# Kernel optimization log

Measured on AMD Instinct MI355X. Metric: run time of the kernel, lower is better.

## Reference

```python
import jax, jax.numpy as jnp
import numpy as np

DIM = 16
HID = 128
B = 1024
STEPS = 10  # RK4 steps in differentiable_forward


def setup_inputs() -> dict:
    key = jax.random.key(0)
    ks = jax.random.split(key, 8)

    def lin(k, fan_in, fan_out):
        return jax.random.normal(k, (fan_in, fan_out), jnp.float32) / np.float32(np.sqrt(fan_in))

    W0 = lin(ks[0], DIM + 1, HID)
    W1 = lin(ks[1], HID, HID)
    W2 = lin(ks[2], HID, HID)
    W3 = lin(ks[3], HID, HID)
    W4 = lin(ks[4], HID, DIM)
    b0 = jnp.zeros((HID,), jnp.float32)
    b1 = jnp.zeros((HID,), jnp.float32)
    b2 = jnp.zeros((HID,), jnp.float32)
    b3 = jnp.zeros((HID,), jnp.float32)
    b4 = jnp.zeros((DIM,), jnp.float32)
    x = jax.random.normal(ks[5], (B, DIM), jnp.float32)
    x_star = jax.random.normal(ks[6], (B, DIM), jnp.float32)
    return dict(x=x, x_star=x_star, W0=W0, b0=b0, W1=W1, b1=b1,
                W2=W2, b2=b2, W3=W3, b3=b3, W4=W4, b4=b4)


def reference(x, x_star, W0, b0, W1, b1, W2, b2, W3, b3, W4, b4):
    dtype = x.dtype

    def vel(t, z):
        # z: [..., DIM]; append scalar time channel -> [..., DIM+1]
        tcol = jnp.full(z.shape[:-1] + (1,), t, dtype)
        h = jnp.concatenate([z, tcol], axis=-1)
        h = jnp.tanh(h @ W0 + b0)
        h = jnp.tanh(h @ W1 + b1)
        h = jnp.tanh(h @ W2 + b2)
        h = jnp.tanh(h @ W3 + b3)
        return h @ W4 + b4

    def flow(z):
        # RK4 integration of the velocity field from t=0 to t=1 (10 steps)
        dt = 1.0 / STEPS
        for i in range(STEPS):
            t = i * dt
            k1 = vel(t, z)
            k2 = vel(t + 0.5 * dt, z + 0.5 * dt * k1)
            k3 = vel(t + 0.5 * dt, z + 0.5 * dt * k2)
            k4 = vel(t + dt, z + dt * k3)
            z = z + (k1 + 2.0 * k2 + 2.0 * k3 + k4) * (dt / 6.0)
        return z

    n = x.shape[0]
    y_comb = flow(jnp.concatenate([x, x_star], axis=0))
    y, y_star = y_comb[:n], y_comb[n:]

    diff = y - y_star
    norm = jnp.linalg.norm(diff, axis=1, keepdims=True) + 1e-8
    grad_phi_y = diff / norm  # [B, DIM]

    # Per-sample Jacobian J[b, i, j] = d y_i / d x_j (flow is pointwise per row)
    J = jax.vmap(jax.jacfwd(flow))(x)  # [B, DIM, DIM]

    G = jnp.einsum('bij,bik->bjk', J, J)  # J^T J
    G_inv = jnp.linalg.inv(G + 1e-6 * jnp.eye(DIM, dtype=dtype))
    grad_phi_x = jnp.einsum('bij,bi->bj', J, grad_phi_y)  # J^T grad_phi_y
    x_dot = -jnp.einsum('bjk,bk->bj', G_inv, grad_phi_x)
    return x_dot
```

## Files before the change

### kernel.cpp

```cpp
#include <hip/hip_runtime.h>
#include <math.h>

typedef _Float16 half8  __attribute__((ext_vector_type(8)));
typedef _Float16 half4  __attribute__((ext_vector_type(4)));
typedef float    float4v __attribute__((ext_vector_type(4)));

#define NDIM   16
#define HID    128
#define NSTEP  10
#define RPW    2
#define NROWS  48
#define XSTR   136
#define XISTR  40
#define SBS    17

__device__ __forceinline__ float tanh_fast(float v) {
  float e = __expf(2.f * v);
  return 1.f - 2.f * __builtin_amdgcn_rcpf(e + 1.f);
}

template<int CTRL>
__device__ __forceinline__ float qbcast(float v) {
  int i = __builtin_amdgcn_update_dpp(0, __builtin_bit_cast(int, v), CTRL, 0xF, 0xF, true);
  return __builtin_bit_cast(float, i);
}

__device__ __forceinline__ int oneuron(int c) {
  return 32*(c >> 5) + 16*((c >> 2) & 1) + 4*((c >> 3) & 3) + (c & 3);
}

__global__ __launch_bounds__(256, 2)
void flow_ode_kernel(const float* __restrict__ gx,  const float* __restrict__ gxs,
                     const float* __restrict__ W0,  const float* __restrict__ b0,
                     const float* __restrict__ W1,  const float* __restrict__ b1,
                     const float* __restrict__ W2,  const float* __restrict__ b2,
                     const float* __restrict__ W3,  const float* __restrict__ b3,
                     const float* __restrict__ W4,  const float* __restrict__ b4,
                     float* __restrict__ out)
{
  __shared__ __align__(16) _Float16 XT[2][NROWS][XSTR];
  __shared__ __align__(16) _Float16 XI[NROWS][XISTR];
  __shared__ float SbL[NROWS][SBS];

  const int tid  = threadIdx.x;
  const int mi   = tid >> 6;
  const int lane = tid & 63;
  const int q    = lane >> 4;
  const int ln   = lane & 15;
  const int g0   = blockIdx.x * RPW;

  half8 A0[2];
  half8 A1[2][4], A2[2][4], A3[2][4];
  half8 A4[4];
  float bw[4][2][4];
  float b4r[4];

  #pragma unroll
  for (int mt = 0; mt < 2; ++mt) {
    const int m = 16*(2*mi + mt) + ln;
    #pragma unroll
    for (int j = 0; j < 8; ++j) {
      const int k = 8*q + j;
      A0[mt][j] = (k < NDIM+1) ? (_Float16)W0[k*HID + m] : (_Float16)0.f;
    }
    #pragma unroll
    for (int ks = 0; ks < 4; ++ks) {
      #pragma unroll
      for (int j = 0; j < 8; ++j) {
        const int k = oneuron(32*ks + 8*q + j);
        A1[mt][ks][j] = (_Float16)W1[k*HID + m];
        A2[mt][ks][j] = (_Float16)W2[k*HID + m];
        A3[mt][ks][j] = (_Float16)W3[k*HID + m];
      }
    }
  }
  #pragma unroll
  for (int ks = 0; ks < 4; ++ks)
    #pragma unroll
    for (int j = 0; j < 8; ++j)
      A4[ks][j] = (_Float16)W4[oneuron(32*ks + 8*q + j)*NDIM + ln];

  #pragma unroll
  for (int mt = 0; mt < 2; ++mt)
    #pragma unroll
    for (int r = 0; r < 4; ++r) {
      const int m = 16*(2*mi + mt) + 4*q + r;
      bw[0][mt][r] = b0[m];
      bw[1][mt][r] = b1[m];
      bw[2][mt][r] = b2[m];
      bw[3][mt][r] = b3[m];
    }
  #pragma unroll
  for (int r = 0; r < 4; ++r) b4r[r] = b4[4*q + r];

  float sbr[4], sar[4];
  if (mi == 0) {
    const int p = ln & 3;
    const float* src = (p < 2) ? (gx + (g0 + p)*NDIM) : (gxs + (g0 + p - 2)*NDIM);
    #pragma unroll
    for (int r = 0; r < 4; ++r) sbr[r] = src[4*q + r];
  } else {
    #pragma unroll
    for (int r = 0; r < 4; ++r) sbr[r] = (ln == 4*q + r) ? 1.f : 0.f;
  }
  #pragma unroll
  for (int r = 0; r < 4; ++r) sar[r] = 0.f;

  for (int idx = tid; idx < NROWS*32; idx += 256)
    XI[idx >> 5][idx & 31] = (_Float16)0.f;
  __syncthreads();
  if (mi < 3) {
    half4 x4;
    #pragma unroll
    for (int r = 0; r < 4; ++r) x4[r] = (_Float16)sbr[r];
    *(half4*)&XI[mi*16 + ln][4*q] = x4;
  }
  __syncthreads();

  if (blockIdx.x & 1) __builtin_amdgcn_s_sleep(22);

  const float dt = 1.f / NSTEP;

  auto finish = [&](float4v (&D)[2][3], int wb) {
    float ss[2][4];
    half8 hh;
    #pragma unroll
    for (int mt = 0; mt < 2; ++mt)
      #pragma unroll
      for (int r = 0; r < 4; ++r) {
        const float h = tanh_fast(D[mt][0][r]);
        hh[4*mt + r] = (_Float16)h;
        ss[mt][r] = 1.f - h*h;
      }
    *(half8*)&XT[wb][ln][32*mi + 8*q] = hh;
    half8 t1, t2;
    #pragma unroll
    for (int mt = 0; mt < 2; ++mt)
      #pragma unroll
      for (int r = 0; r < 4; ++r) {
        t1[4*mt + r] = (_Float16)(D[mt][1][r] * qbcast<0x00>(ss[mt][r]));
        t2[4*mt + r] = (_Float16)(D[mt][2][r] * qbcast<0x55>(ss[mt][r]));
      }
    *(half8*)&XT[wb][16 + ln][32*mi + 8*q] = t1;
    *(half8*)&XT[wb][32 + ln][32*mi + 8*q] = t2;
    __syncthreads();
  };

  auto mid_layer = [&](const half8 (&A)[2][4], const float (&bb)[2][4], int rb, int wb) {
    float4v D[2][3];
    #pragma unroll
    for (int mt = 0; mt < 2; ++mt)
      #pragma unroll
      for (int nt = 0; nt < 3; ++nt)
        #pragma unroll
        for (int e = 0; e < 4; ++e) D[mt][nt][e] = (nt == 0) ? bb[mt][e] : 0.f;
    #pragma unroll
    for (int ks = 0; ks < 4; ++ks) {
      half8 Bf[3];
      #pragma unroll
      for (int nt = 0; nt < 3; ++nt)
        Bf[nt] = *(const half8*)&XT[rb][nt*16 + ln][32*ks + 8*q];
      #pragma unroll
      for (int nt = 0; nt < 3; ++nt) {
        D[0][nt] = __builtin_amdgcn_mfma_f32_16x16x32_f16(A[0][ks], Bf[nt], D[0][nt], 0, 0, 0);
        D[1][nt] = __builtin_amdgcn_mfma_f32_16x16x32_f16(A[1][ks], Bf[nt], D[1][nt], 0, 0, 0);
      }
    }
    finish(D, wb);
  };

  #pragma unroll 1
  for (int step = 0; step < NSTEP; ++step) {
    const float t0 = step * dt;
    #pragma unroll
    for (int stage = 0; stage < 4; ++stage) {
      {
        float4v D[2][3];
        #pragma unroll
        for (int mt = 0; mt < 2; ++mt)
          #pragma unroll
          for (int nt = 0; nt < 3; ++nt)
            #pragma unroll
            for (int e = 0; e < 4; ++e) D[mt][nt][e] = (nt == 0) ? bw[0][mt][e] : 0.f;
        half8 Bf[3];
        #pragma unroll
        for (int nt = 0; nt < 3; ++nt)
          Bf[nt] = *(const half8*)&XI[nt*16 + ln][8*q];
        #pragma unroll
        for (int nt = 0; nt < 3; ++nt) {
          D[0][nt] = __builtin_amdgcn_mfma_f32_16x16x32_f16(A0[0], Bf[nt], D[0][nt], 0, 0, 0);
          D[1][nt] = __builtin_amdgcn_mfma_f32_16x16x32_f16(A0[1], Bf[nt], D[1][nt], 0, 0, 0);
        }
        finish(D, 0);
      }
      mid_layer(A1, bw[1], 0, 1);
      mid_layer(A2, bw[2], 1, 0);
      mid_layer(A3, bw[3], 0, 1);
      {
        if (mi < 3) {
          float4v Da;
          #pragma unroll
          for (int e = 0; e < 4; ++e) Da[e] = (mi == 0) ? b4r[e] : 0.f;
          #pragma unroll
          for (int ks = 0; ks < 4; ++ks) {
            half8 Ba = *(const half8*)&XT[1][mi*16 + ln][32*ks + 8*q];
            Da = __builtin_amdgcn_mfma_f32_16x16x32_f16(A4[ks], Ba, Da, 0, 0, 0);
          }
          const float c_s = (stage < 2) ? 0.5f*dt : dt;
          half4 xn;
          if (stage < 3) {
            const float w_s = (stage == 0) ? 1.f : 2.f;
            #pragma unroll
            for (int r = 0; r < 4; ++r) {
              sar[r] += w_s * Da[r];
              xn[r] = (_Float16)(sbr[r] + c_s * Da[r]);
            }
          } else {
            #pragma unroll
            for (int r = 0; r < 4; ++r) {
              const float nb = sbr[r] + (dt * (1.f/6.f)) * (sar[r] + Da[r]);
              sbr[r] = nb;
              sar[r] = 0.f;
              xn[r] = (_Float16)nb;
            }
          }
          *(half4*)&XI[mi*16 + ln][4*q] = xn;
          if (mi == 0 && q == 0)
            XI[ln][16] = (_Float16)(t0 + ((stage < 2) ? 0.5f*dt : dt));
        }
        __syncthreads();
      }
    }
  }

  if (mi < 3) {
    #pragma unroll
    for (int r = 0; r < 4; ++r)
      SbL[mi*16 + ln][4*q + r] = sbr[r];
  }
  __syncthreads();

  if (mi < RPW) {
    const int p    = mi;
    const int jj   = ln;
    const int base = lane & 48;
    float c[NDIM], gv[NDIM], G[NDIM];
    #pragma unroll
    for (int i = 0; i < NDIM; ++i) c[i] = SbL[16 + 16*p + jj][i];
    float n2 = 0.f;
    #pragma unroll
    for (int i = 0; i < NDIM; ++i) {
      gv[i] = SbL[p][i] - SbL[2 + p][i];
      n2 += gv[i]*gv[i];
    }
    const float rinv = 1.f / (sqrtf(n2) + 1e-8f);
    float rhs = 0.f;
    #pragma unroll
    for (int i = 0; i < NDIM; ++i) rhs += c[i] * gv[i];
    rhs *= rinv;
    #pragma unroll
    for (int k = 0; k < NDIM; ++k) {
      float acc = (k == jj) ? 1e-6f : 0.f;
      #pragma unroll
      for (int i = 0; i < NDIM; ++i)
        acc += c[i] * __shfl(c[i], base + k, 64);
      G[k] = acc;
    }
    #pragma unroll
    for (int k = 0; k < NDIM-1; ++k) {
      const float piv  = __shfl(G[k], base + k, 64);
      const float prhs = __shfl(rhs,  base + k, 64);
      const float f = (jj > k) ? G[k] / piv : 0.f;
      #pragma unroll
      for (int cc = k; cc < NDIM; ++cc)
        G[cc] -= f * __shfl(G[cc], base + k, 64);
      rhs -= f * prhs;
    }
    float sol = 0.f;
    #pragma unroll
    for (int k = NDIM-1; k >= 0; --k) {
      const float piv = __shfl(G[k], base + k, 64);
      const float pr  = __shfl(rhs,  base + k, 64);
      const float xk  = pr / piv;
      if (jj == k) sol = xk;
      if (jj <  k) rhs -= G[k] * xk;
    }
    if (lane < NDIM)
      out[(g0 + p)*NDIM + jj] = -sol;
  }
}

extern "C" void kernel_launch(void* const* d_in, const int* in_sizes, int n_in,
                              void* d_out, int out_size, void* d_ws, size_t ws_size,
                              hipStream_t stream) {
  (void)in_sizes; (void)n_in; (void)d_ws; (void)ws_size; (void)out_size;
  flow_ode_kernel<<<dim3(512), dim3(256), 0, stream>>>(
      (const float*)d_in[0],  (const float*)d_in[1],
      (const float*)d_in[2],  (const float*)d_in[3],
      (const float*)d_in[4],  (const float*)d_in[5],
      (const float*)d_in[6],  (const float*)d_in[7],
      (const float*)d_in[8],  (const float*)d_in[9],
      (const float*)d_in[10], (const float*)d_in[11],
      (float*)d_out);
}
```

Measured before the change: 238.1 us.

## Halve block to two waves, each wave computing two neuron slices

Each block now runs 128 threads (two wavefronts) instead of four. Each wave holds weights for two 32-neuron slices and issues twice as many MFMAs per layer, and the per-wave state vectors are doubled to match. This reduces barrier participants and per-block LDS contention, and lets the B-fragment LDS reads be shared across more MFMAs. In exchange it roughly doubles weight registers per wave (launch bounds set to 128,1), which may cause spills or lower occupancy and serialises more work per wave.

```diff
diff --git a/kernel.cpp b/kernel.cpp
--- a/kernel.cpp
+++ b/kernel.cpp
@@ -29,7 +29,7 @@
   return 32*(c >> 5) + 16*((c >> 2) & 1) + 4*((c >> 3) & 3) + (c & 3);
 }
 
-__global__ __launch_bounds__(256, 2)
+__global__ __launch_bounds__(128, 1)
 void flow_ode_kernel(const float* __restrict__ gx,  const float* __restrict__ gxs,
                      const float* __restrict__ W0,  const float* __restrict__ b0,
                      const float* __restrict__ W1,  const float* __restrict__ b1,
@@ -49,28 +49,40 @@
   const int ln   = lane & 15;
   const int g0   = blockIdx.x * RPW;
 
-  half8 A0[2];
-  half8 A1[2][4], A2[2][4], A3[2][4];
+  half8 A0[2][2];
+  half8 A1[2][2][4], A2[2][2][4], A3[2][2][4];
   half8 A4[4];
-  float bw[4][2][4];
+  float bw[4][2][2][4];
   float b4r[4];
 
   #pragma unroll
-  for (int mt = 0; mt < 2; ++mt) {
-    const int m = 16*(2*mi + mt) + ln;
-    #pragma unroll
-    for (int j = 0; j < 8; ++j) {
-      const int k = 8*q + j;
-      A0[mt][j] = (k < NDIM+1) ? (_Float16)W0[k*HID + m] : (_Float16)0.f;
-    }
-    #pragma unroll
-    for (int ks = 0; ks < 4; ++ks) {
+  for (int h = 0; h < 2; ++h) {
+    const int v = 2*mi + h;
+    #pragma unroll
+    for (int mt = 0; mt < 2; ++mt) {
+      const int m = 16*(2*v + mt) + ln;
       #pragma unroll
       for (int j = 0; j < 8; ++j) {
-        const int k = oneuron(32*ks + 8*q + j);
-        A1[mt][ks][j] = (_Float16)W1[k*HID + m];
-        A2[mt][ks][j] = (_Float16)W2[k*HID + m];
-        A3[mt][ks][j] = (_Float16)W3[k*HID + m];
+        const int k = 8*q + j;
+        A0[h][mt][j] = (k < NDIM+1) ? (_Float16)W0[k*HID + m] : (_Float16)0.f;
+      }
+      #pragma unroll
+      for (int ks = 0; ks < 4; ++ks) {
+        #pragma unroll
+        for (int j = 0; j < 8; ++j) {
+          const int k = oneuron(32*ks + 8*q + j);
+          A1[h][mt][ks][j] = (_Float16)W1[k*HID + m];
+          A2[h][mt][ks][j] = (_Float16)W2[k*HID + m];
+          A3[h][mt][ks][j] = (_Float16)W3[k*HID + m];
+        }
+      }
+      #pragma unroll
+      for (int r = 0; r < 4; ++r) {
+        const int mm = 16*(2*v + mt) + 4*q + r;
+        bw[0][h][mt][r] = b0[mm];
+        bw[1][h][mt][r] = b1[mm];
+        bw[2][h][mt][r] = b2[mm];
+        bw[3][h][mt][r] = b3[mm];
       }
     }
   }
@@ -79,41 +91,42 @@
     #pragma unroll
     for (int j = 0; j < 8; ++j)
       A4[ks][j] = (_Float16)W4[oneuron(32*ks + 8*q + j)*NDIM + ln];
-
-  #pragma unroll
-  for (int mt = 0; mt < 2; ++mt)
-    #pragma unroll
-    for (int r = 0; r < 4; ++r) {
-      const int m = 16*(2*mi + mt) + 4*q + r;
-      bw[0][mt][r] = b0[m];
-      bw[1][mt][r] = b1[m];
-      bw[2][mt][r] = b2[m];
-      bw[3][mt][r] = b3[m];
-    }
   #pragma unroll
   for (int r = 0; r < 4; ++r) b4r[r] = b4[4*q + r];
 
-  float sbr[4], sar[4];
+  float sbr[2][4], sar[2][4];
   if (mi == 0) {
     const int p = ln & 3;
     const float* src = (p < 2) ? (gx + (g0 + p)*NDIM) : (gxs + (g0 + p - 2)*NDIM);
     #pragma unroll
-    for (int r = 0; r < 4; ++r) sbr[r] = src[4*q + r];
+    for (int r = 0; r < 4; ++r) {
+      sbr[0][r] = src[4*q + r];
+      sbr[1][r] = (ln == 4*q + r) ? 1.f : 0.f;
+    }
   } else {
     #pragma unroll
-    for (int r = 0; r < 4; ++r) sbr[r] = (ln == 4*q + r) ? 1.f : 0.f;
-  }
-  #pragma unroll
-  for (int r = 0; r < 4; ++r) sar[r] = 0.f;
-
-  for (int idx = tid; idx < NROWS*32; idx += 256)
+    for (int r = 0; r < 4; ++r) {
+      sbr[0][r] = (ln == 4*q + r) ? 1.f : 0.f;
+      sbr[1][r] = 0.f;
+    }
+  }
+  #pragma unroll
+  for (int h = 0; h < 2; ++h)
+    #pragma unroll
+    for (int r = 0; r < 4; ++r) sar[h][r] = 0.f;
+
+  for (int idx = tid; idx < NROWS*32; idx += 128)
     XI[idx >> 5][idx & 31] = (_Float16)0.f;
   __syncthreads();
-  if (mi < 3) {
-    half4 x4;
-    #pragma unroll
-    for (int r = 0; r < 4; ++r) x4[r] = (_Float16)sbr[r];
-    *(half4*)&XI[mi*16 + ln][4*q] = x4;
+  #pragma unroll
+  for (int h = 0; h < 2; ++h) {
+    const int v = 2*mi + h;
+    if (v < 3) {
+      half4 x4;
+      #pragma unroll
+      for (int r = 0; r < 4; ++r) x4[r] = (_Float16)sbr[h][r];
+      *(half4*)&XI[v*16 + ln][4*q] = x4;
+    }
   }
   __syncthreads();
 
@@ -121,39 +134,45 @@
 
   const float dt = 1.f / NSTEP;
 
-  auto finish = [&](float4v (&D)[2][3], int wb) {
-    float ss[2][4];
-    half8 hh;
-    #pragma unroll
-    for (int mt = 0; mt < 2; ++mt)
-      #pragma unroll
-      for (int r = 0; r < 4; ++r) {
-        const float h = tanh_fast(D[mt][0][r]);
-        hh[4*mt + r] = (_Float16)h;
-        ss[mt][r] = 1.f - h*h;
-      }
-    *(half8*)&XT[wb][ln][32*mi + 8*q] = hh;
-    half8 t1, t2;
-    #pragma unroll
-    for (int mt = 0; mt < 2; ++mt)
-      #pragma unroll
-      for (int r = 0; r < 4; ++r) {
-        t1[4*mt + r] = (_Float16)(D[mt][1][r] * qbcast<0x00>(ss[mt][r]));
-        t2[4*mt + r] = (_Float16)(D[mt][2][r] * qbcast<0x55>(ss[mt][r]));
-      }
-    *(half8*)&XT[wb][16 + ln][32*mi + 8*q] = t1;
-    *(half8*)&XT[wb][32 + ln][32*mi + 8*q] = t2;
+  auto finish = [&](float4v (&D)[2][2][3], int wb) {
+    #pragma unroll
+    for (int h = 0; h < 2; ++h) {
+      const int v = 2*mi + h;
+      float ss[2][4];
+      half8 hh;
+      #pragma unroll
+      for (int mt = 0; mt < 2; ++mt)
+        #pragma unroll
+        for (int r = 0; r < 4; ++r) {
+          const float hv = tanh_fast(D[h][mt][0][r]);
+          hh[4*mt + r] = (_Float16)hv;
+          ss[mt][r] = 1.f - hv*hv;
+        }
+      *(half8*)&XT[wb][ln][32*v + 8*q] = hh;
+      half8 t1, t2;
+      #pragma unroll
+      for (int mt = 0; mt < 2; ++mt)
+        #pragma unroll
+        for (int r = 0; r < 4; ++r) {
+          t1[4*mt + r] = (_Float16)(D[h][mt][1][r] * qbcast<0x00>(ss[mt][r]));
+          t2[4*mt + r] = (_Float16)(D[h][mt][2][r] * qbcast<0x55>(ss[mt][r]));
+        }
+      *(half8*)&XT[wb][16 + ln][32*v + 8*q] = t1;
+      *(half8*)&XT[wb][32 + ln][32*v + 8*q] = t2;
+    }
     __syncthreads();
   };
 
-  auto mid_layer = [&](const half8 (&A)[2][4], const float (&bb)[2][4], int rb, int wb) {
-    float4v D[2][3];
-    #pragma unroll
-    for (int mt = 0; mt < 2; ++mt)
-      #pragma unroll
-      for (int nt = 0; nt < 3; ++nt)
-        #pragma unroll
-        for (int e = 0; e < 4; ++e) D[mt][nt][e] = (nt == 0) ? bb[mt][e] : 0.f;
+  auto mid_layer = [&](const half8 (&A)[2][2][4], const float (&bb)[2][2][4], int rb, int wb) {
+    float4v D[2][2][3];
+    #pragma unroll
+    for (int h = 0; h < 2; ++h)
+      #pragma unroll
+      for (int mt = 0; mt < 2; ++mt)
+        #pragma unroll
+        for (int nt = 0; nt < 3; ++nt)
+          #pragma unroll
+          for (int e = 0; e < 4; ++e) D[h][mt][nt][e] = (nt == 0) ? bb[h][mt][e] : 0.f;
     #pragma unroll
     for (int ks = 0; ks < 4; ++ks) {
       half8 Bf[3];
@@ -161,10 +180,12 @@
       for (int nt = 0; nt < 3; ++nt)
         Bf[nt] = *(const half8*)&XT[rb][nt*16 + ln][32*ks + 8*q];
       #pragma unroll
-      for (int nt = 0; nt < 3; ++nt) {
-        D[0][nt] = __builtin_amdgcn_mfma_f32_16x16x32_f16(A[0][ks], Bf[nt], D[0][nt], 0, 0, 0);
-        D[1][nt] = __builtin_amdgcn_mfma_f32_16x16x32_f16(A[1][ks], Bf[nt], D[1][nt], 0, 0, 0);
-      }
+      for (int h = 0; h < 2; ++h)
+        #pragma unroll
+        for (int mt = 0; mt < 2; ++mt)
+          #pragma unroll
+          for (int nt = 0; nt < 3; ++nt)
+            D[h][mt][nt] = __builtin_amdgcn_mfma_f32_16x16x32_f16(A[h][mt][ks], Bf[nt], D[h][mt][nt], 0, 0, 0);
     }
     finish(D, wb);
   };
@@ -175,72 +196,84 @@
     #pragma unroll
     for (int stage = 0; stage < 4; ++stage) {
       {
-        float4v D[2][3];
-        #pragma unroll
-        for (int mt = 0; mt < 2; ++mt)
+        float4v D[2][2][3];
+        #pragma unroll
+        for (int h = 0; h < 2; ++h)
           #pragma unroll
-          for (int nt = 0; nt < 3; ++nt)
+          for (int mt = 0; mt < 2; ++mt)
             #pragma unroll
-            for (int e = 0; e < 4; ++e) D[mt][nt][e] = (nt == 0) ? bw[0][mt][e] : 0.f;
+            for (int nt = 0; nt < 3; ++nt)
+              #pragma unroll
+              for (int e = 0; e < 4; ++e) D[h][mt][nt][e] = (nt == 0) ? bw[0][h][mt][e] : 0.f;
         half8 Bf[3];
         #pragma unroll
         for (int nt = 0; nt < 3; ++nt)
           Bf[nt] = *(const half8*)&XI[nt*16 + ln][8*q];
         #pragma unroll
-        for (int nt = 0; nt < 3; ++nt) {
-          D[0][nt] = __builtin_amdgcn_mfma_f32_16x16x32_f16(A0[0], Bf[nt], D[0][nt], 0, 0, 0);
-          D[1][nt] = __builtin_amdgcn_mfma_f32_16x16x32_f16(A0[1], Bf[nt], D[1][nt], 0, 0, 0);
-        }
+        for (int h = 0; h < 2; ++h)
+          #pragma unroll
+          for (int mt = 0; mt < 2; ++mt)
+            #pragma unroll
+            for (int nt = 0; nt < 3; ++nt)
+              D[h][mt][nt] = __builtin_amdgcn_mfma_f32_16x16x32_f16(A0[h][mt], Bf[nt], D[h][mt][nt], 0, 0, 0);
         finish(D, 0);
       }
       mid_layer(A1, bw[1], 0, 1);
       mid_layer(A2, bw[2], 1, 0);
       mid_layer(A3, bw[3], 0, 1);
       {
-        if (mi < 3) {
-          float4v Da;
-          #pragma unroll
-          for (int e = 0; e < 4; ++e) Da[e] = (mi == 0) ? b4r[e] : 0.f;
-          #pragma unroll
-          for (int ks = 0; ks < 4; ++ks) {
-            half8 Ba = *(const half8*)&XT[1][mi*16 + ln][32*ks + 8*q];
-            Da = __builtin_amdgcn_mfma_f32_16x16x32_f16(A4[ks], Ba, Da, 0, 0, 0);
+        #pragma unroll
+        for (int h = 0; h < 2; ++h) {
+          const int v = 2*mi + h;
+          if (v < 3) {
+            float4v Da;
+            #pragma unroll
+            for (int e = 0; e < 4; ++e) Da[e] = (v == 0) ? b4r[e] : 0.f;
+            #pragma unroll
+            for (int ks = 0; ks < 4; ++ks) {
+              half8 Ba = *(const half8*)&XT[1][v*16 + ln][32*ks + 8*q];
+              Da = __builtin_amdgcn_mfma_f32_16x16x32_f16(A4[ks], Ba, Da, 0, 0, 0);
+            }
+            const float c_s = (stage < 2) ? 0.5f*dt : dt;
+            half4 xn;
+            if (stage < 3) {
+              const float w_s = (stage == 0) ? 1.f : 2.f;
+              #pragma unroll
+              for (int r = 0; r < 4; ++r) {
+                sar[h][r] += w_s * Da[r];
+                xn[r] = (_Float16)(sbr[h][r] + c_s * Da[r]);
+              }
+            } else {
+              #pragma unroll
+              for (int r = 0; r < 4; ++r) {
+                const float nb = sbr[h][r] + (dt * (1.f/6.f)) * (sar[h][r] + Da[r]);
+                sbr[h][r] = nb;
+                sar[h][r] = 0.f;
+                xn[r] = (_Float16)nb;
+              }
+            }
+            *(half4*)&XI[v*16 + ln][4*q] = xn;
+            if (v == 0 && q == 0)
+              XI[ln][16] = (_Float16)(t0 + c_s);
           }
-          const float c_s = (stage < 2) ? 0.5f*dt : dt;
-          half4 xn;
-          if (stage < 3) {
-            const float w_s = (stage == 0) ? 1.f : 2.f;
-            #pragma unroll
-            for (int r = 0; r < 4; ++r) {
-              sar[r] += w_s * Da[r];
-              xn[r] = (_Float16)(sbr[r] + c_s * Da[r]);
-            }
-          } else {
-            #pragma unroll
-            for (int r = 0; r < 4; ++r) {
-              const float nb = sbr[r] + (dt * (1.f/6.f)) * (sar[r] + Da[r]);
-              sbr[r] = nb;
-              sar[r] = 0.f;
-              xn[r] = (_Float16)nb;
-            }
-          }
-          *(half4*)&XI[mi*16 + ln][4*q] = xn;
-          if (mi == 0 && q == 0)
-            XI[ln][16] = (_Float16)(t0 + ((stage < 2) ? 0.5f*dt : dt));
         }
         __syncthreads();
       }
     }
   }
 
-  if (mi < 3) {
-    #pragma unroll
-    for (int r = 0; r < 4; ++r)
-      SbL[mi*16 + ln][4*q + r] = sbr[r];
+  #pragma unroll
+  for (int h = 0; h < 2; ++h) {
+    const int v = 2*mi + h;
+    if (v < 3) {
+      #pragma unroll
+      for (int r = 0; r < 4; ++r)
+        SbL[v*16 + ln][4*q + r] = sbr[h][r];
+    }
   }
   __syncthreads();
 
-  if (mi < RPW) {
+  {
     const int p    = mi;
     const int jj   = ln;
     const int base = lane & 48;
@@ -294,7 +327,7 @@
                               void* d_out, int out_size, void* d_ws, size_t ws_size,
                               hipStream_t stream) {
   (void)in_sizes; (void)n_in; (void)d_ws; (void)ws_size; (void)out_size;
-  flow_ode_kernel<<<dim3(512), dim3(256), 0, stream>>>(
+  flow_ode_kernel<<<dim3(512), dim3(128), 0, stream>>>(
       (const float*)d_in[0],  (const float*)d_in[1],
       (const float*)d_in[2],  (const float*)d_in[3],
       (const float*)d_in[4],  (const float*)d_in[5],
```

Measured after the change: 297.3 us. +24.8%, slower.
